# Kernel tuning notes

Measured on AMD Instinct MI355X. Metric: run time of the kernel, lower is better.

Reference implementation:

```python
import jax, jax.numpy as jnp
import numpy as np

MASKED = True


def setup_inputs() -> dict:
    key = jax.random.key(0)
    kq, kk, kv = jax.random.split(key, 3)
    shape = (4, 16, 2048, 64)  # [B, H, S, d]
    q = jax.random.normal(kq, shape, dtype=jnp.float32)
    k = jax.random.normal(kk, shape, dtype=jnp.float32)
    v = jax.random.normal(kv, shape, dtype=jnp.float32)
    return {"q": q, "k": k, "v": v}


def reference(q, k, v):
    d = k.shape[-1]
    scale = 1.0 / jnp.sqrt(jnp.asarray(d, dtype=q.dtype))
    # [B, H, S, S]
    att = jnp.einsum("bhqd,bhkd->bhqk", q, k) * scale
    if MASKED:
        # Faithful to torch source: tril of the scores, then mask where zero
        tri = jnp.tril(att)
        att = jnp.where(tri == 0, -jnp.inf, att)
    att = jax.nn.softmax(att, axis=-1)
    return jnp.einsum("bhqk,bhkd->bhqd", att, v)
```

## Files before the change

kernel.cpp:

```cpp
#include <hip/hip_runtime.h>
#include <hip/hip_bf16.h>

typedef __attribute__((ext_vector_type(8)))  short bf16x8;
typedef __attribute__((ext_vector_type(4)))  float f32x4;
typedef __attribute__((ext_vector_type(16))) float f32x16;
typedef unsigned short ushort_t;

#define S_LEN 2048
#define D_DIM 64
#define FIXED_M 14.0f

#if __has_builtin(__builtin_amdgcn_exp2f)
#define EXP2(x) __builtin_amdgcn_exp2f(x)
#else
#define EXP2(x) __expf((x) * 0.6931471805599453f)
#endif

__device__ __forceinline__ short f2bf(float f) {
  union { float f; unsigned u; } x; x.f = f;
  unsigned r = x.u + 0x7fffu + ((x.u >> 16) & 1u);
  return (short)(r >> 16);
}

__device__ __forceinline__ unsigned cvtpk_bf16(float lo, float hi) {
  unsigned r;
  asm("v_cvt_pk_bf16_f32 %0, %1, %2" : "=v"(r) : "v"(lo), "v"(hi));
  return r;
}

__device__ __forceinline__ void pl32swap(unsigned& a, unsigned& b) {
  asm volatile("v_permlane32_swap_b32 %0, %1" : "+v"(a), "+v"(b));
}

__device__ __forceinline__ void gl_lds16(const ushort_t* g, ushort_t* l) {
  __builtin_amdgcn_global_load_lds(
      (const __attribute__((address_space(1))) unsigned*)g,
      (__attribute__((address_space(3))) unsigned*)l, 16, 0, 0);
}

__global__ void prep_kernel(const float* __restrict__ Kf, const float* __restrict__ Vf,
                            ushort_t* __restrict__ Kb, ushort_t* __restrict__ Vt) {
  if (blockIdx.x < 2048) {
    const long n8 = (long)64 * S_LEN * D_DIM / 8;
    long i = (long)blockIdx.x * blockDim.x + threadIdx.x;
    const long stride = (long)2048 * blockDim.x;
    for (; i < n8; i += stride) {
      const float4* p = (const float4*)(Kf + i * 8);
      float4 a = p[0], b = p[1];
      bf16x8 t;
      t[0]=f2bf(a.x); t[1]=f2bf(a.y); t[2]=f2bf(a.z); t[3]=f2bf(a.w);
      t[4]=f2bf(b.x); t[5]=f2bf(b.y); t[6]=f2bf(b.z); t[7]=f2bf(b.w);
      *(bf16x8*)(Kb + i * 8) = t;
    }
  } else {
    const int bid = blockIdx.x - 2048;
    const int h  = bid >> 5;
    const int s0 = (bid & 31) * 64;
    const float* Vh = Vf + (size_t)h * S_LEN * D_DIM;
    ushort_t* Vth   = Vt + (size_t)h * D_DIM * S_LEN;
    __shared__ float tile[64][65];
    const int r  = threadIdx.x >> 2;
    const int c4 = (threadIdx.x & 3) * 16;
#pragma unroll
    for (int j = 0; j < 16; j += 4) {
      float4 x = *(const float4*)(Vh + (size_t)(s0 + r) * D_DIM + c4 + j);
      tile[r][c4 + j + 0] = x.x; tile[r][c4 + j + 1] = x.y;
      tile[r][c4 + j + 2] = x.z; tile[r][c4 + j + 3] = x.w;
    }
    __syncthreads();
    bf16x8 o0, o1;
#pragma unroll
    for (int j = 0; j < 8; ++j) o0[j] = f2bf(tile[c4 + j][r]);
#pragma unroll
    for (int j = 0; j < 8; ++j) o1[j] = f2bf(tile[c4 + 8 + j][r]);
    *(bf16x8*)(Vth + (size_t)r * S_LEN + s0 + c4)     = o0;
    *(bf16x8*)(Vth + (size_t)r * S_LEN + s0 + c4 + 8) = o1;
  }
}

__global__ __launch_bounds__(256, 2)
void flash32_kernel(const float* __restrict__ Qf, const ushort_t* __restrict__ Kb,
                    const ushort_t* __restrict__ Vt, float* __restrict__ Og) {
  const int tid = threadIdx.x;
  const int l   = tid & 63;
  const int wv  = tid >> 6;
  const int hi  = l >> 5;
  const int l31 = l & 31;
  const int l7  = l & 7;
  const int l8  = l >> 3;

  const int bid  = blockIdx.x;
  const int r6   = bid & 63;
  const int head = (r6 & 7) * 8 + (r6 >> 3);
  const int p    = bid >> 6;
  const int qhiQ = 15 - p;
  const int qloQ = p;

  const float*    Qh = Qf + (size_t)head * S_LEN * D_DIM;
  const ushort_t* Kh = Kb + (size_t)head * S_LEN * D_DIM;
  const ushort_t* Vh = Vt + (size_t)head * D_DIM * S_LEN;
  float*          Oh = Og + (size_t)head * S_LEN * D_DIM;

  __shared__ ushort_t smK[2][64 * 64];
  __shared__ ushort_t smV[2][64 * 64];

  const int swsrc = (l7 ^ l8) * 8;
  const int rb    = l31 * 64;

#define STAGE_K(T, B) do {                                                 \
    const int kvk_ = (T) * 64;                                             \
    _Pragma("unroll")                                                      \
    for (int u_ = 0; u_ < 2; ++u_) {                                       \
      const int idx_ = wv * 2 + u_;                                        \
      const int row_ = idx_ * 8 + l8;                                      \
      gl_lds16(Kh + (size_t)(kvk_ + row_) * 64 + swsrc,                    \
               &smK[B][idx_ * 512]);                                       \
    }                                                                      \
  } while (0)

#define STAGE_V(T, B) do {                                                 \
    const int kvv_ = (T) * 64;                                             \
    _Pragma("unroll")                                                      \
    for (int u_ = 0; u_ < 2; ++u_) {                                       \
      const int idx_ = wv * 2 + u_;                                        \
      const int d_ = idx_ * 8 + l8;                                        \
      gl_lds16(Vh + (size_t)d_ * S_LEN + kvv_ + swsrc,                     \
               &smV[B][idx_ * 512]);                                       \
    }                                                                      \
  } while (0)

#define VMCNT0() asm volatile("s_waitcnt vmcnt(0)" ::: "memory")
#define BAR()    __builtin_amdgcn_s_barrier()

#define QKT(S0, S1, KB) do {                                               \
    _Pragma("unroll")                                                      \
    for (int i = 0; i < 16; ++i) { S0[i] = -FIXED_M; S1[i] = -FIXED_M; }   \
    const ushort_t* kb_ = smK[KB];                                         \
    _Pragma("unroll")                                                      \
    for (int ks = 0; ks < 4; ++ks) {                                       \
      const int ch = ((ks * 2 + hi) ^ l7) * 8;                             \
      bf16x8 a0 = *(const bf16x8*)(kb_ + rb + ch);                         \
      bf16x8 a1 = *(const bf16x8*)(kb_ + 2048 + rb + ch);                  \
      S0 = __builtin_amdgcn_mfma_f32_32x32x16_bf16(a0, qf[ks], S0, 0, 0, 0); \
      S1 = __builtin_amdgcn_mfma_f32_32x32x16_bf16(a1, qf[ks], S1, 0, 0, 0); \
    }                                                                      \
  } while (0)

#define SOFTMAX(S0, S1, KV0) do {                                          \
    if ((KV0) + 63 > qminw) {                                              \
      _Pragma("unroll")                                                    \
      for (int r = 0; r < 16; ++r) {                                       \
        const int crow = (r & 3) + 8 * (r >> 2) + 4 * hi;                  \
        if ((KV0) + crow > qrow)      S0[r] = -INFINITY;                   \
        if ((KV0) + 32 + crow > qrow) S1[r] = -INFINITY;                   \
      }                                                                    \
    }                                                                      \
    _Pragma("unroll")                                                      \
    for (int i = 0; i < 16; ++i) S0[i] = EXP2(S0[i]);                      \
    _Pragma("unroll")                                                      \
    for (int i = 0; i < 16; ++i) S1[i] = EXP2(S1[i]);                      \
    float b8[8];                                                           \
    _Pragma("unroll")                                                      \
    for (int i = 0; i < 8; ++i)                                            \
      b8[i] = (S0[i] + S0[i+8]) + (S1[i] + S1[i+8]);                       \
    _Pragma("unroll")                                                      \
    for (int i = 0; i < 4; ++i) b8[i] += b8[i+4];                          \
    l_run += (b8[0] + b8[2]) + (b8[1] + b8[3]);                            \
    _Pragma("unroll")                                                      \
    for (int ks = 0; ks < 4; ++ks) {                                       \
      const int r0 = (ks & 1) * 8;                                         \
      unsigned w0, w1, w2, w3;                                             \
      if (ks < 2) {                                                        \
        w0 = cvtpk_bf16(S0[r0+0], S0[r0+1]); w2 = cvtpk_bf16(S0[r0+4], S0[r0+5]); \
        w1 = cvtpk_bf16(S0[r0+2], S0[r0+3]); w3 = cvtpk_bf16(S0[r0+6], S0[r0+7]); \
      } else {                                                             \
        w0 = cvtpk_bf16(S1[r0+0], S1[r0+1]); w2 = cvtpk_bf16(S1[r0+4], S1[r0+5]); \
        w1 = cvtpk_bf16(S1[r0+2], S1[r0+3]); w3 = cvtpk_bf16(S1[r0+6], S1[r0+7]); \
      }                                                                    \
      pl32swap(w0, w2); pl32swap(w1, w3);                                  \
      union { unsigned u[4]; bf16x8 v; } pu_;                              \
      pu_.u[0] = w0; pu_.u[1] = w1; pu_.u[2] = w2; pu_.u[3] = w3;          \
      pw[ks] = pu_.v;                                                      \
    }                                                                      \
  } while (0)

#define PV(VB) do {                                                        \
    const ushort_t* vb_ = smV[VB];                                         \
    _Pragma("unroll")                                                      \
    for (int ks = 0; ks < 4; ++ks) {                                       \
      const int ch = ((ks * 2 + hi) ^ l7) * 8;                             \
      bf16x8 va  = *(const bf16x8*)(vb_ + rb + ch);                        \
      bf16x8 vB2 = *(const bf16x8*)(vb_ + 2048 + rb + ch);                 \
      accA = __builtin_amdgcn_mfma_f32_32x32x16_bf16(va,  pw[ks], accA, 0, 0, 0); \
      accB = __builtin_amdgcn_mfma_f32_32x32x16_bf16(vB2, pw[ks], accB, 0, 0, 0); \
    }                                                                      \
  } while (0)

  for (int seg = 0; seg < 2; ++seg) {
    const int qidx = seg ? qloQ : qhiQ;
    const int q0   = qidx * 128;
    const int nt   = 2 * qidx + 2;

    const int qrow  = q0 + wv * 32 + l31;
    const int qminw = q0 + wv * 32;

    if (seg) BAR();

    STAGE_K(0, 0);
    STAGE_V(0, 0);
    STAGE_K(1, 1);

    bf16x8 qf[4];
    {
      const float sc = 0.125f * 1.44269504089f;
      const float* qp = Qh + (size_t)qrow * D_DIM + 8 * hi;
#pragma unroll
      for (int ks = 0; ks < 4; ++ks) {
        float4 x = *(const float4*)(qp + ks * 16);
        float4 y = *(const float4*)(qp + ks * 16 + 4);
        bf16x8 t;
        t[0]=f2bf(x.x*sc); t[1]=f2bf(x.y*sc);
        t[2]=f2bf(x.z*sc); t[3]=f2bf(x.w*sc);
        t[4]=f2bf(y.x*sc); t[5]=f2bf(y.y*sc);
        t[6]=f2bf(y.z*sc); t[7]=f2bf(y.w*sc);
        qf[ks] = t;
      }
    }

    f32x16 accA, accB, sA0, sA1, sB0, sB1;
#pragma unroll
    for (int i = 0; i < 16; ++i) { accA[i] = 0.f; accB[i] = 0.f; }
    float l_run = 0.f;
    bf16x8 pw[4];

    VMCNT0();
    BAR();
    QKT(sA0, sA1, 0);

    for (int t = 0; t + 2 < nt; t += 2) {
      VMCNT0(); BAR();
      STAGE_K(t + 2, 0);
      STAGE_V(t + 1, 1);
      QKT(sB0, sB1, 1);
      SOFTMAX(sA0, sA1, t * 64);
      PV(0);
      VMCNT0(); BAR();
      STAGE_K(t + 3, 1);
      STAGE_V(t + 2, 0);
      QKT(sA0, sA1, 0);
      SOFTMAX(sB0, sB1, (t + 1) * 64);
      PV(1);
    }
    {
      const int t = nt - 2;
      VMCNT0(); BAR();
      STAGE_V(t + 1, 1);
      QKT(sB0, sB1, 1);
      SOFTMAX(sA0, sA1, t * 64);
      PV(0);
      VMCNT0(); BAR();
      SOFTMAX(sB0, sB1, (t + 1) * 64);
      PV(1);
    }

    l_run += __shfl_xor(l_run, 32, 64);
    const float inv = 1.0f / l_run;
    float* op = Oh + (size_t)qrow * D_DIM + 4 * hi;
#pragma unroll
    for (int m4 = 0; m4 < 4; ++m4) {
      float4 a = { accA[4*m4+0]*inv, accA[4*m4+1]*inv,
                   accA[4*m4+2]*inv, accA[4*m4+3]*inv };
      *(float4*)(op + 8 * m4) = a;
      float4 b = { accB[4*m4+0]*inv, accB[4*m4+1]*inv,
                   accB[4*m4+2]*inv, accB[4*m4+3]*inv };
      *(float4*)(op + 32 + 8 * m4) = b;
    }
  }

#undef STAGE_K
#undef STAGE_V
#undef VMCNT0
#undef BAR
#undef QKT
#undef SOFTMAX
#undef PV
}

#define BQ 64
#define BK 64
#define LDK 72
#define LDP 72

__device__ __forceinline__ unsigned pack_bf(float lo, float hi) {
  return (unsigned)(unsigned short)f2bf(lo) |
         ((unsigned)(unsigned short)f2bf(hi) << 16);
}

__global__ __launch_bounds__(256, 2)
void flash_fwd_kernel(const float* __restrict__ Qg, const float* __restrict__ Kg,
                      const float* __restrict__ Vg, float* __restrict__ Og) {
  const int tid  = threadIdx.x;
  const int lane = tid & 63;
  const int wv   = tid >> 6;
  const int grp  = lane >> 4;
  const int l16  = lane & 15;
  const int bid = blockIdx.x;
  const int qb  = 31 - (bid & 31);
  const int bh  = bid >> 5;
  const int q0  = qb * BQ;
  const size_t hoff = (size_t)bh * S_LEN * D_DIM;
  const float* Qh = Qg + hoff;
  const float* Kh = Kg + hoff;
  const float* Vh = Vg + hoff;
  float*       Oh = Og + hoff;
  __shared__ short sK [BK][LDK];
  __shared__ short sVT[D_DIM][LDP];
  __shared__ short sP [4][16][LDP];
  bf16x8 qf[2];
  {
    const float* qrow = Qh + (size_t)(q0 + wv*16 + l16) * D_DIM + grp*8;
#pragma unroll
    for (int kc = 0; kc < 2; ++kc) {
      float4 a = *reinterpret_cast<const float4*>(qrow + kc*32);
      float4 b = *reinterpret_cast<const float4*>(qrow + kc*32 + 4);
      bf16x8 t;
      t[0]=f2bf(a.x*0.125f); t[1]=f2bf(a.y*0.125f);
      t[2]=f2bf(a.z*0.125f); t[3]=f2bf(a.w*0.125f);
      t[4]=f2bf(b.x*0.125f); t[5]=f2bf(b.y*0.125f);
      t[6]=f2bf(b.z*0.125f); t[7]=f2bf(b.w*0.125f);
      qf[kc] = t;
    }
  }
  f32x4 acc[4];
#pragma unroll
  for (int nb = 0; nb < 4; ++nb) acc[nb] = (f32x4){0.f, 0.f, 0.f, 0.f};
  float m_i[4] = {-INFINITY, -INFINITY, -INFINITY, -INFINITY};
  float l_i[4] = {0.f, 0.f, 0.f, 0.f};
  const int srow = tid >> 2;
  const int scb  = tid & 3;
  for (int kt = 0; kt <= qb; ++kt) {
    const int kv0 = kt * BK;
    __syncthreads();
    {
      const float* src = Kh + (size_t)(kv0 + srow) * D_DIM + scb*16;
      float4 x0 = *reinterpret_cast<const float4*>(src);
      float4 x1 = *reinterpret_cast<const float4*>(src + 4);
      float4 x2 = *reinterpret_cast<const float4*>(src + 8);
      float4 x3 = *reinterpret_cast<const float4*>(src + 12);
      bf16x8 lo, hi;
      lo[0]=f2bf(x0.x); lo[1]=f2bf(x0.y); lo[2]=f2bf(x0.z); lo[3]=f2bf(x0.w);
      lo[4]=f2bf(x1.x); lo[5]=f2bf(x1.y); lo[6]=f2bf(x1.z); lo[7]=f2bf(x1.w);
      hi[0]=f2bf(x2.x); hi[1]=f2bf(x2.y); hi[2]=f2bf(x2.z); hi[3]=f2bf(x2.w);
      hi[4]=f2bf(x3.x); hi[5]=f2bf(x3.y); hi[6]=f2bf(x3.z); hi[7]=f2bf(x3.w);
      *reinterpret_cast<bf16x8*>(&sK[srow][scb*16])     = lo;
      *reinterpret_cast<bf16x8*>(&sK[srow][scb*16 + 8]) = hi;
    }
    {
      const float* src = Vh + (size_t)(kv0 + scb*16) * D_DIM + srow;
      bf16x8 lo, hi;
#pragma unroll
      for (int j = 0; j < 8; ++j) lo[j] = f2bf(src[(size_t)j * D_DIM]);
#pragma unroll
      for (int j = 0; j < 8; ++j) hi[j] = f2bf(src[(size_t)(j + 8) * D_DIM]);
      *reinterpret_cast<bf16x8*>(&sVT[srow][scb*16])     = lo;
      *reinterpret_cast<bf16x8*>(&sVT[srow][scb*16 + 8]) = hi;
    }
    __syncthreads();
    f32x4 sc[4];
#pragma unroll
    for (int nb = 0; nb < 4; ++nb) {
      f32x4 c = (f32x4){0.f, 0.f, 0.f, 0.f};
#pragma unroll
      for (int kc = 0; kc < 2; ++kc) {
        bf16x8 kf = *reinterpret_cast<const bf16x8*>(&sK[nb*16 + l16][kc*32 + grp*8]);
        c = __builtin_amdgcn_mfma_f32_16x16x32_bf16(qf[kc], kf, c, 0, 0, 0);
      }
      sc[nb] = c;
    }
    const bool diag = (kt == qb);
#pragma unroll
    for (int r = 0; r < 4; ++r) {
      const int qi = wv*16 + grp*4 + r;
      float s0 = sc[0][r], s1 = sc[1][r], s2 = sc[2][r], s3 = sc[3][r];
      if (diag) {
        if (l16 +  0 > qi) s0 = -INFINITY;
        if (l16 + 16 > qi) s1 = -INFINITY;
        if (l16 + 32 > qi) s2 = -INFINITY;
        if (l16 + 48 > qi) s3 = -INFINITY;
      }
      float mx = fmaxf(fmaxf(s0, s1), fmaxf(s2, s3));
#pragma unroll
      for (int off = 8; off; off >>= 1)
        mx = fmaxf(mx, __shfl_xor(mx, off, 64));
      const float mn    = fmaxf(m_i[r], mx);
      const float alpha = __expf(m_i[r] - mn);
      const float p0 = __expf(s0 - mn);
      const float p1 = __expf(s1 - mn);
      const float p2 = __expf(s2 - mn);
      const float p3 = __expf(s3 - mn);
      float rs = (p0 + p1) + (p2 + p3);
#pragma unroll
      for (int off = 8; off; off >>= 1)
        rs += __shfl_xor(rs, off, 64);
      l_i[r] = l_i[r] * alpha + rs;
      m_i[r] = mn;
      acc[0][r] *= alpha; acc[1][r] *= alpha;
      acc[2][r] *= alpha; acc[3][r] *= alpha;
      const float n0 = __shfl_xor(p0, 1, 64);
      const float n1 = __shfl_xor(p1, 1, 64);
      const float n2 = __shfl_xor(p2, 1, 64);
      const float n3 = __shfl_xor(p3, 1, 64);
      if (!(lane & 1)) {
        const int prow = grp*4 + r;
        unsigned* base = reinterpret_cast<unsigned*>(&sP[wv][prow][l16]);
        base[0]  = pack_bf(p0, n0);
        base[8]  = pack_bf(p1, n1);
        base[16] = pack_bf(p2, n2);
        base[24] = pack_bf(p3, n3);
      }
    }
    bf16x8 pf[2];
#pragma unroll
    for (int kc = 0; kc < 2; ++kc)
      pf[kc] = *reinterpret_cast<const bf16x8*>(&sP[wv][l16][kc*32 + grp*8]);
#pragma unroll
    for (int nb = 0; nb < 4; ++nb) {
#pragma unroll
      for (int kc = 0; kc < 2; ++kc) {
        bf16x8 vf = *reinterpret_cast<const bf16x8*>(&sVT[l16 + 16*nb][kc*32 + grp*8]);
        acc[nb] = __builtin_amdgcn_mfma_f32_16x16x32_bf16(pf[kc], vf, acc[nb], 0, 0, 0);
      }
    }
  }
#pragma unroll
  for (int r = 0; r < 4; ++r) {
    const float inv = 1.0f / l_i[r];
    float* orow = Oh + (size_t)(q0 + wv*16 + grp*4 + r) * D_DIM + l16;
#pragma unroll
    for (int nb = 0; nb < 4; ++nb)
      orow[nb*16] = acc[nb][r] * inv;
  }
}

extern "C" void kernel_launch(void* const* d_in, const int* in_sizes, int n_in,
                              void* d_out, int out_size, void* d_ws, size_t ws_size,
                              hipStream_t stream) {
  (void)n_in; (void)out_size;
  const float* q = (const float*)d_in[0];
  const float* k = (const float*)d_in[1];
  const float* v = (const float*)d_in[2];
  float* o = (float*)d_out;
  const int bh = in_sizes[0] / (S_LEN * D_DIM);
  const size_t elems = (size_t)bh * S_LEN * D_DIM;

  if (ws_size >= elems * 2 * 2 && bh == 64) {
    ushort_t* Kb = (ushort_t*)d_ws;
    ushort_t* Vt = Kb + elems;
    prep_kernel<<<4096, 256, 0, stream>>>(k, v, Kb, Vt);
    flash32_kernel<<<bh * 8, 256, 0, stream>>>(q, Kb, Vt, o);
  } else {
    flash_fwd_kernel<<<bh * (S_LEN / BQ), 256, 0, stream>>>(q, k, v, o);
  }
}
```

Baseline: 72.86 us.

## Process 64 query rows per wave with 2 waves per block

Halves the block to two waves, each handling two 32-row query sub-tiles, so every K and V fragment read from LDS feeds twice as many MFMAs. The software pipeline is simplified to a single-stage prefetch of the next K/V tile with one barrier per iteration, replacing the interleaved QK/softmax overlap. This cuts LDS read traffic per FLOP but doubles accumulator registers and reduces the waves per CU available for latency hiding. It also drops the overlap between QK^T of the next tile and softmax of the current one.

```diff
diff --git a/kernel.cpp b/kernel.cpp
--- a/kernel.cpp
+++ b/kernel.cpp
@@ -78,7 +78,7 @@
   }
 }
 
-__global__ __launch_bounds__(256, 2)
+__global__ __launch_bounds__(128, 2)
 void flash32_kernel(const float* __restrict__ Qf, const ushort_t* __restrict__ Kb,
                     const ushort_t* __restrict__ Vt, float* __restrict__ Og) {
   const int tid = threadIdx.x;
@@ -110,8 +110,8 @@
 #define STAGE_K(T, B) do {                                                 \
     const int kvk_ = (T) * 64;                                             \
     _Pragma("unroll")                                                      \
-    for (int u_ = 0; u_ < 2; ++u_) {                                       \
-      const int idx_ = wv * 2 + u_;                                        \
+    for (int u_ = 0; u_ < 4; ++u_) {                                       \
+      const int idx_ = wv * 4 + u_;                                        \
       const int row_ = idx_ * 8 + l8;                                      \
       gl_lds16(Kh + (size_t)(kvk_ + row_) * 64 + swsrc,                    \
                &smK[B][idx_ * 512]);                                       \
@@ -121,8 +121,8 @@
 #define STAGE_V(T, B) do {                                                 \
     const int kvv_ = (T) * 64;                                             \
     _Pragma("unroll")                                                      \
-    for (int u_ = 0; u_ < 2; ++u_) {                                       \
-      const int idx_ = wv * 2 + u_;                                        \
+    for (int u_ = 0; u_ < 4; ++u_) {                                       \
+      const int idx_ = wv * 4 + u_;                                        \
       const int d_ = idx_ * 8 + l8;                                        \
       gl_lds16(Vh + (size_t)d_ * S_LEN + kvv_ + swsrc,                     \
                &smV[B][idx_ * 512]);                                       \
@@ -132,27 +132,32 @@
 #define VMCNT0() asm volatile("s_waitcnt vmcnt(0)" ::: "memory")
 #define BAR()    __builtin_amdgcn_s_barrier()
 
-#define QKT(S0, S1, KB) do {                                               \
-    _Pragma("unroll")                                                      \
-    for (int i = 0; i < 16; ++i) { S0[i] = -FIXED_M; S1[i] = -FIXED_M; }   \
+#define QKT(KB) do {                                                       \
+    _Pragma("unroll")                                                      \
+    for (int i = 0; i < 16; ++i) {                                         \
+      sA0[i] = -FIXED_M; sA1[i] = -FIXED_M;                                \
+      sB0[i] = -FIXED_M; sB1[i] = -FIXED_M;                                \
+    }                                                                      \
     const ushort_t* kb_ = smK[KB];                                         \
     _Pragma("unroll")                                                      \
     for (int ks = 0; ks < 4; ++ks) {                                       \
       const int ch = ((ks * 2 + hi) ^ l7) * 8;                             \
       bf16x8 a0 = *(const bf16x8*)(kb_ + rb + ch);                         \
       bf16x8 a1 = *(const bf16x8*)(kb_ + 2048 + rb + ch);                  \
-      S0 = __builtin_amdgcn_mfma_f32_32x32x16_bf16(a0, qf[ks], S0, 0, 0, 0); \
-      S1 = __builtin_amdgcn_mfma_f32_32x32x16_bf16(a1, qf[ks], S1, 0, 0, 0); \
+      sA0 = __builtin_amdgcn_mfma_f32_32x32x16_bf16(a0, qfA[ks], sA0, 0, 0, 0); \
+      sA1 = __builtin_amdgcn_mfma_f32_32x32x16_bf16(a1, qfA[ks], sA1, 0, 0, 0); \
+      sB0 = __builtin_amdgcn_mfma_f32_32x32x16_bf16(a0, qfB[ks], sB0, 0, 0, 0); \
+      sB1 = __builtin_amdgcn_mfma_f32_32x32x16_bf16(a1, qfB[ks], sB1, 0, 0, 0); \
     }                                                                      \
   } while (0)
 
-#define SOFTMAX(S0, S1, KV0) do {                                          \
-    if ((KV0) + 63 > qminw) {                                              \
+#define SOFTMAX(S0, S1, KV0, QMINW, QROW, LRUN, PW) do {                   \
+    if ((KV0) + 63 > (QMINW)) {                                            \
       _Pragma("unroll")                                                    \
       for (int r = 0; r < 16; ++r) {                                       \
         const int crow = (r & 3) + 8 * (r >> 2) + 4 * hi;                  \
-        if ((KV0) + crow > qrow)      S0[r] = -INFINITY;                   \
-        if ((KV0) + 32 + crow > qrow) S1[r] = -INFINITY;                   \
+        if ((KV0) + crow > (QROW))      S0[r] = -INFINITY;                 \
+        if ((KV0) + 32 + crow > (QROW)) S1[r] = -INFINITY;                 \
       }                                                                    \
     }                                                                      \
     _Pragma("unroll")                                                      \
@@ -165,7 +170,7 @@
       b8[i] = (S0[i] + S0[i+8]) + (S1[i] + S1[i+8]);                       \
     _Pragma("unroll")                                                      \
     for (int i = 0; i < 4; ++i) b8[i] += b8[i+4];                          \
-    l_run += (b8[0] + b8[2]) + (b8[1] + b8[3]);                            \
+    LRUN += (b8[0] + b8[2]) + (b8[1] + b8[3]);                             \
     _Pragma("unroll")                                                      \
     for (int ks = 0; ks < 4; ++ks) {                                       \
       const int r0 = (ks & 1) * 8;                                         \
@@ -180,7 +185,7 @@
       pl32swap(w0, w2); pl32swap(w1, w3);                                  \
       union { unsigned u[4]; bf16x8 v; } pu_;                              \
       pu_.u[0] = w0; pu_.u[1] = w1; pu_.u[2] = w2; pu_.u[3] = w3;          \
-      pw[ks] = pu_.v;                                                      \
+      PW[ks] = pu_.v;                                                      \
     }                                                                      \
   } while (0)
 
@@ -191,8 +196,10 @@
       const int ch = ((ks * 2 + hi) ^ l7) * 8;                             \
       bf16x8 va  = *(const bf16x8*)(vb_ + rb + ch);                        \
       bf16x8 vB2 = *(const bf16x8*)(vb_ + 2048 + rb + ch);                 \
-      accA = __builtin_amdgcn_mfma_f32_32x32x16_bf16(va,  pw[ks], accA, 0, 0, 0); \
-      accB = __builtin_amdgcn_mfma_f32_32x32x16_bf16(vB2, pw[ks], accB, 0, 0, 0); \
+      accA0 = __builtin_amdgcn_mfma_f32_32x32x16_bf16(va,  pwA[ks], accA0, 0, 0, 0); \
+      accB0 = __builtin_amdgcn_mfma_f32_32x32x16_bf16(vB2, pwA[ks], accB0, 0, 0, 0); \
+      accA1 = __builtin_amdgcn_mfma_f32_32x32x16_bf16(va,  pwB[ks], accA1, 0, 0, 0); \
+      accB1 = __builtin_amdgcn_mfma_f32_32x32x16_bf16(vB2, pwB[ks], accB1, 0, 0, 0); \
     }                                                                      \
   } while (0)
 
@@ -201,79 +208,85 @@
     const int q0   = qidx * 128;
     const int nt   = 2 * qidx + 2;
 
-    const int qrow  = q0 + wv * 32 + l31;
-    const int qminw = q0 + wv * 32;
-
-    if (seg) BAR();
+    const int qbase  = q0 + wv * 64;
+    const int qminwA = qbase;
+    const int qrowA  = qbase + l31;
+    const int qminwB = qbase + 32;
+    const int qrowB  = qminwB + l31;
 
     STAGE_K(0, 0);
     STAGE_V(0, 0);
-    STAGE_K(1, 1);
-
-    bf16x8 qf[4];
+
+    bf16x8 qfA[4], qfB[4];
     {
       const float sc = 0.125f * 1.44269504089f;
-      const float* qp = Qh + (size_t)qrow * D_DIM + 8 * hi;
+      const float* qpA = Qh + (size_t)qrowA * D_DIM + 8 * hi;
+      const float* qpB = Qh + (size_t)qrowB * D_DIM + 8 * hi;
 #pragma unroll
       for (int ks = 0; ks < 4; ++ks) {
-        float4 x = *(const float4*)(qp + ks * 16);
-        float4 y = *(const float4*)(qp + ks * 16 + 4);
+        float4 x = *(const float4*)(qpA + ks * 16);
+        float4 y = *(const float4*)(qpA + ks * 16 + 4);
         bf16x8 t;
         t[0]=f2bf(x.x*sc); t[1]=f2bf(x.y*sc);
         t[2]=f2bf(x.z*sc); t[3]=f2bf(x.w*sc);
         t[4]=f2bf(y.x*sc); t[5]=f2bf(y.y*sc);
         t[6]=f2bf(y.z*sc); t[7]=f2bf(y.w*sc);
-        qf[ks] = t;
-      }
-    }
-
-    f32x16 accA, accB, sA0, sA1, sB0, sB1;
-#pragma unroll
-    for (int i = 0; i < 16; ++i) { accA[i] = 0.f; accB[i] = 0.f; }
-    float l_run = 0.f;
-    bf16x8 pw[4];
+        qfA[ks] = t;
+        float4 u = *(const float4*)(qpB + ks * 16);
+        float4 v = *(const float4*)(qpB + ks * 16 + 4);
+        bf16x8 s;
+        s[0]=f2bf(u.x*sc); s[1]=f2bf(u.y*sc);
+        s[2]=f2bf(u.z*sc); s[3]=f2bf(u.w*sc);
+        s[4]=f2bf(v.x*sc); s[5]=f2bf(v.y*sc);
+        s[6]=f2bf(v.z*sc); s[7]=f2bf(v.w*sc);
+        qfB[ks] = s;
+      }
+    }
+
+    f32x16 accA0, accB0, accA1, accB1, sA0, sA1, sB0, sB1;
+#pragma unroll
+    for (int i = 0; i < 16; ++i) {
+      accA0[i] = 0.f; accB0[i] = 0.f; accA1[i] = 0.f; accB1[i] = 0.f;
+    }
+    float l_runA = 0.f, l_runB = 0.f;
+    bf16x8 pwA[4], pwB[4];
 
     VMCNT0();
     BAR();
-    QKT(sA0, sA1, 0);
-
-    for (int t = 0; t + 2 < nt; t += 2) {
-      VMCNT0(); BAR();
-      STAGE_K(t + 2, 0);
-      STAGE_V(t + 1, 1);
-      QKT(sB0, sB1, 1);
-      SOFTMAX(sA0, sA1, t * 64);
-      PV(0);
-      VMCNT0(); BAR();
-      STAGE_K(t + 3, 1);
-      STAGE_V(t + 2, 0);
-      QKT(sA0, sA1, 0);
-      SOFTMAX(sB0, sB1, (t + 1) * 64);
-      PV(1);
-    }
-    {
-      const int t = nt - 2;
-      VMCNT0(); BAR();
-      STAGE_V(t + 1, 1);
-      QKT(sB0, sB1, 1);
-      SOFTMAX(sA0, sA1, t * 64);
-      PV(0);
-      VMCNT0(); BAR();
-      SOFTMAX(sB0, sB1, (t + 1) * 64);
-      PV(1);
-    }
-
-    l_run += __shfl_xor(l_run, 32, 64);
-    const float inv = 1.0f / l_run;
-    float* op = Oh + (size_t)qrow * D_DIM + 4 * hi;
+
+    for (int t = 0; t < nt; ++t) {
+      if (t + 1 < nt) {
+        STAGE_K(t + 1, (t + 1) & 1);
+        STAGE_V(t + 1, (t + 1) & 1);
+      }
+      QKT(t & 1);
+      SOFTMAX(sA0, sA1, t * 64, qminwA, qrowA, l_runA, pwA);
+      SOFTMAX(sB0, sB1, t * 64, qminwB, qrowB, l_runB, pwB);
+      PV(t & 1);
+      VMCNT0();
+      BAR();
+    }
+
+    l_runA += __shfl_xor(l_runA, 32, 64);
+    l_runB += __shfl_xor(l_runB, 32, 64);
+    const float invA = 1.0f / l_runA;
+    const float invB = 1.0f / l_runB;
+    float* opA = Oh + (size_t)qrowA * D_DIM + 4 * hi;
+    float* opB = Oh + (size_t)qrowB * D_DIM + 4 * hi;
 #pragma unroll
     for (int m4 = 0; m4 < 4; ++m4) {
-      float4 a = { accA[4*m4+0]*inv, accA[4*m4+1]*inv,
-                   accA[4*m4+2]*inv, accA[4*m4+3]*inv };
-      *(float4*)(op + 8 * m4) = a;
-      float4 b = { accB[4*m4+0]*inv, accB[4*m4+1]*inv,
-                   accB[4*m4+2]*inv, accB[4*m4+3]*inv };
-      *(float4*)(op + 32 + 8 * m4) = b;
+      float4 a = { accA0[4*m4+0]*invA, accA0[4*m4+1]*invA,
+                   accA0[4*m4+2]*invA, accA0[4*m4+3]*invA };
+      *(float4*)(opA + 8 * m4) = a;
+      float4 b = { accB0[4*m4+0]*invA, accB0[4*m4+1]*invA,
+                   accB0[4*m4+2]*invA, accB0[4*m4+3]*invA };
+      *(float4*)(opA + 32 + 8 * m4) = b;
+      float4 c = { accA1[4*m4+0]*invB, accA1[4*m4+1]*invB,
+                   accA1[4*m4+2]*invB, accA1[4*m4+3]*invB };
+      *(float4*)(opB + 8 * m4) = c;
+      float4 d = { accB1[4*m4+0]*invB, accB1[4*m4+1]*invB,
+                   accB1[4*m4+2]*invB, accB1[4*m4+3]*invB };
+      *(float4*)(opB + 32 + 8 * m4) = d;
     }
   }
 
@@ -457,7 +470,7 @@
     ushort_t* Kb = (ushort_t*)d_ws;
     ushort_t* Vt = Kb + elems;
     prep_kernel<<<4096, 256, 0, stream>>>(k, v, Kb, Vt);
-    flash32_kernel<<<bh * 8, 256, 0, stream>>>(q, Kb, Vt, o);
+    flash32_kernel<<<bh * 8, 128, 0, stream>>>(q, Kb, Vt, o);
   } else {
     flash_fwd_kernel<<<bh * (S_LEN / BQ), 256, 0, stream>>>(q, k, v, o);
   }
```

Result: slower. 105.3 us (+44.5%).
